# Performance work log

Measured on AMD Instinct MI355X. Metric: run time of the kernel, lower is better.

The kernel has to match this reference:

```python
import jax, jax.numpy as jnp
import numpy as np

B, T, H = 32, 2048, 1024
NEG = -1e9


def setup_inputs() -> dict:
    key = jax.random.key(0)
    ks = jax.random.split(key, 10)
    s = 1.0 / np.sqrt(H)
    return {
        "query": jax.random.normal(ks[0], (B, T, H), dtype=jnp.float32),
        "key_": jax.random.normal(ks[1], (B, T, H), dtype=jnp.float32),
        "value": jax.random.normal(ks[2], (B, T, H), dtype=jnp.float32),
        "lengths": jax.random.randint(ks[3], (B,), 1, T + 1),
        "Wq": jax.random.uniform(ks[4], (H, H), jnp.float32, -s, s),
        "bq": jax.random.uniform(ks[5], (H,), jnp.float32, -s, s),
        "Wk": jax.random.uniform(ks[6], (H, H), jnp.float32, -s, s),
        "bk": jax.random.uniform(ks[7], (H,), jnp.float32, -s, s),
        "Wz": jax.random.uniform(ks[8], (1, H), jnp.float32, -s, s),
        "bz": jax.random.uniform(ks[9], (1,), jnp.float32, -s, s),
    }


def reference(query, key_, value, lengths, Wq, bq, Wk, bk, Wz, bz):
    # projections: [B,T,H] @ [H,H]^T
    q = jnp.einsum("bth,oh->bto", query, Wq) + bq
    k = jnp.einsum("bth,oh->bto", key_, Wk) + bk
    # additive score -> [B,T,1]
    score = jnp.einsum("bth,oh->bto", jnp.tanh(q + k), Wz) + bz
    # mask positions t >= lengths[b]
    t_idx = jnp.arange(T)[None, :, None]  # [1,T,1]
    mask = t_idx >= lengths[:, None, None]  # [B,T,1]
    score = jnp.where(mask, NEG, score)
    att_weights = jax.nn.softmax(score, axis=1)  # [B,T,1]
    # weights^T [B,1,T] @ value [B,T,H] -> [B,1,H]
    att_value = jnp.einsum("bti,bth->bih", att_weights, value)
    return att_value, att_weights
```

## Files before the change

### kernel.cpp

```cpp
#include <hip/hip_runtime.h>
#include <hip/hip_bf16.h>

constexpr int TSEQ  = 2048;
constexpr int HDIM  = 1024;
constexpr int BATCH = 32;
constexpr int NPART = 16;
constexpr long ROWS = (long)BATCH * TSEQ;

constexpr int GBM = 256, GBN = 256, GBK = 64;
constexpr int GNT = (2 * HDIM) / GBK;

constexpr int BM = 128, BN = 128, BK = 64;
constexpr int NT = (2 * HDIM) / BK;

typedef __attribute__((ext_vector_type(8))) short bf16x8;
typedef __attribute__((ext_vector_type(8))) unsigned short u16x8;
typedef __attribute__((ext_vector_type(4))) float f32x4;

__device__ __forceinline__ unsigned short f2bf(float f) {
    union { float f; unsigned int u; } v; v.f = f;
    unsigned int r = v.u + 0x7FFFu + ((v.u >> 16) & 1u);
    return (unsigned short)(r >> 16);
}

__device__ __forceinline__ void gload16(const unsigned short* g, unsigned short* l) {
    __builtin_amdgcn_global_load_lds(
        (__attribute__((address_space(1))) void*)(g),
        (__attribute__((address_space(3))) void*)(l), 16, 0, 0);
}

__device__ __forceinline__ float fast_tanh(float x) {
    float e = __expf(2.0f * x);
    return 1.0f - 2.0f * __builtin_amdgcn_rcpf(e + 1.0f);
}

__global__ void convert_kernel(const float* __restrict__ q, const float* __restrict__ k,
                               const float* __restrict__ wq, const float* __restrict__ wk,
                               const int* __restrict__ lengths,
                               unsigned short* __restrict__ qb, unsigned short* __restrict__ kb,
                               unsigned short* __restrict__ wqb, unsigned short* __restrict__ wkb) {
    const long GQ = (ROWS * HDIM) / 8;
    const long GW = ((long)HDIM * HDIM) / 8;
    const long TOTAL = 2 * GQ + 2 * GW;
    const long stride = (long)gridDim.x * blockDim.x;
    for (long i = (long)blockIdx.x * blockDim.x + threadIdx.x; i < TOTAL; i += stride) {
        const float* src; unsigned short* dst; long off;
        if (i < 2 * GQ) {
            off = (i < GQ) ? i : i - GQ;
            const int row = (int)(off >> 7);
            if ((row & (TSEQ - 1)) >= lengths[row >> 11]) continue;
            src = (i < GQ) ? q : k;  dst = (i < GQ) ? qb : kb;
        } else if (i < 2 * GQ + GW) { src = wq; dst = wqb; off = i - 2 * GQ; }
        else                        { src = wk; dst = wkb; off = i - 2 * GQ - GW; }
        float4 v0 = *(const float4*)(src + off * 8);
        float4 v1 = *(const float4*)(src + off * 8 + 4);
        u16x8 o;
        o[0] = f2bf(v0.x); o[1] = f2bf(v0.y); o[2] = f2bf(v0.z); o[3] = f2bf(v0.w);
        o[4] = f2bf(v1.x); o[5] = f2bf(v1.y); o[6] = f2bf(v1.z); o[7] = f2bf(v1.w);
        *(u16x8*)(dst + off * 8) = o;
    }
}

__global__ __launch_bounds__(512, 2)
void score_gemm_256(const unsigned short* __restrict__ qb, const unsigned short* __restrict__ kb,
                    const unsigned short* __restrict__ wqb, const unsigned short* __restrict__ wkb,
                    const float* __restrict__ bq, const float* __restrict__ bk,
                    const float* __restrict__ Wz, const int* __restrict__ lengths,
                    float* __restrict__ scorePartial) {
    __shared__ unsigned short As[2 * 2 * 256 * 32];
    __shared__ unsigned short Bs[2 * 2 * 256 * 32];

    const int tid  = threadIdx.x;
    const int lane = tid & 63;
    const int wid  = tid >> 6;
    const int wr   = wid >> 2;
    const int wc   = wid & 3;

    const int lid = ((int)blockIdx.x & 7) * 128 + ((int)blockIdx.x >> 3);
    const int nb  = lid & 3;
    const int mb  = lid >> 2;
    const long rowBase = (long)mb * GBM;
    const int  colBase = nb * GBN;

    if ((int)(rowBase & (TSEQ - 1)) >= lengths[(int)(rowBase >> 11)]) return;

    const int frow = lane & 15;
    const int cs16 = (((lane >> 4) ^ ((frow >> 1) & 3)) << 4);
    const int sc8  = ((tid & 3) ^ ((tid >> 3) & 3)) * 8;

    f32x4 acc[8][4];
#pragma unroll
    for (int i = 0; i < 8; ++i)
#pragma unroll
        for (int j = 0; j < 4; ++j) acc[i][j] = (f32x4){0.f, 0.f, 0.f, 0.f};

    auto stage_half = [&](int n) {
        if (n >= 4 * GNT) return;
        const int tn   = n >> 2;
        const int part = n & 3;
        const int kh   = part >> 1;
        const int isB  = part & 1;
        const int kglob = tn * GBK + kh * 32;
        const unsigned short* src = (tn < 16) ? (isB ? wqb : qb) : (isB ? wkb : kb);
        const int ksrc = (tn < 16) ? kglob : (kglob - HDIM);
        const long rbase = isB ? (long)colBase : rowBase;
        unsigned short* lds = (isB ? Bs : As) + (tn & 1) * 16384 + kh * 8192;
#pragma unroll
        for (int j = 0; j < 2; ++j) {
            const int row = j * 128 + (tid >> 2);
            gload16(src + (rbase + row) * (long)HDIM + ksrc + sc8,
                    lds + j * 4096 + (tid << 3));
        }
    };

    bf16x8 afr[4], bfr[4];
    auto ldA = [&](int d, int kh, int mh) {
        const char* p = (const char*)As + d * 32768 + kh * 16384;
#pragma unroll
        for (int mi = 0; mi < 4; ++mi) {
            const int row = wr * 128 + (mh * 4 + mi) * 16 + frow;
            afr[mi] = *(const bf16x8*)(p + row * 64 + cs16);
        }
    };
    auto ldB = [&](int d, int kh) {
        const char* p = (const char*)Bs + d * 32768 + kh * 16384;
#pragma unroll
        for (int ni = 0; ni < 4; ++ni) {
            const int row = wc * 64 + ni * 16 + frow;
            bfr[ni] = *(const bf16x8*)(p + row * 64 + cs16);
        }
    };

#pragma unroll
    for (int n = 0; n < 6; ++n) stage_half(n);
    asm volatile("s_waitcnt vmcnt(4)" ::: "memory");
    __builtin_amdgcn_s_barrier();

    for (int t = 0; t < GNT; ++t) {
        const int d = t & 1;
#pragma unroll
        for (int q = 0; q < 4; ++q) {
            const int kh = q >> 1, mh = q & 1;
            if (mh == 0) ldB(d, kh);
            ldA(d, kh, mh);
            stage_half(4 * t + q + 6);
            __builtin_amdgcn_s_barrier();
            asm volatile("s_waitcnt lgkmcnt(0)" ::: "memory");
            __builtin_amdgcn_sched_barrier(0);
            __builtin_amdgcn_s_setprio(1);
#pragma unroll
            for (int mi = 0; mi < 4; ++mi)
#pragma unroll
                for (int ni = 0; ni < 4; ++ni)
                    acc[mh * 4 + mi][ni] = __builtin_amdgcn_mfma_f32_16x16x32_bf16(
                        afr[mi], bfr[ni], acc[mh * 4 + mi][ni], 0, 0, 0);
            __builtin_amdgcn_s_setprio(0);
            if (q == 3) {
                if (t < GNT - 2)       asm volatile("s_waitcnt vmcnt(4)" ::: "memory");
                else if (t == GNT - 2) asm volatile("s_waitcnt vmcnt(0)" ::: "memory");
            }
            __builtin_amdgcn_s_barrier();
        }
    }

    float bias[4], wz[4];
#pragma unroll
    for (int ni = 0; ni < 4; ++ni) {
        const int o = colBase + wc * 64 + ni * 16 + frow;
        bias[ni] = bq[o] + bk[o];
        wz[ni]   = Wz[o];
    }
#pragma unroll
    for (int mi = 0; mi < 8; ++mi) {
#pragma unroll
        for (int j = 0; j < 4; ++j) {
            float p = 0.f;
#pragma unroll
            for (int ni = 0; ni < 4; ++ni)
                p += fast_tanh(acc[mi][ni][j] + bias[ni]) * wz[ni];
#pragma unroll
            for (int off = 1; off < 16; off <<= 1) p += __shfl_xor(p, off);
            if (frow == 0) {
                long r = rowBase + wr * 128 + mi * 16 + (lane >> 4) * 4 + j;
                scorePartial[r * NPART + nb * 4 + wc] = p;
            }
        }
    }
}

__global__ __launch_bounds__(256, 2)
void score_gemm_fused(const float* __restrict__ query, const float* __restrict__ key_,
                      const float* __restrict__ Wq, const float* __restrict__ Wk,
                      const float* __restrict__ bq, const float* __restrict__ bk,
                      const float* __restrict__ Wz, const int* __restrict__ lengths,
                      float* __restrict__ scorePartial) {
    __shared__ unsigned short As[2][BM * BK];
    __shared__ unsigned short Bs[2][BN * BK];
    const int tid  = threadIdx.x;
    const int lane = tid & 63;
    const int wid  = tid >> 6;
    const int wr   = wid >> 1, wc = wid & 1;
    const int bid = blockIdx.x;
    const int nb  = bid & 7;
    const int mb  = bid >> 3;
    const long rowBase = (long)mb * BM;
    const int  colBase = nb * BN;
    if ((int)(rowBase & (TSEQ - 1)) >= lengths[(int)(rowBase >> 11)]) return;
    const int srow = tid >> 4;
    const int sc   = tid & 15;
    const int rA  = wr * 64 + (lane & 15);
    const int rB  = wc * 64 + (lane & 15);
    const int swz = (lane & 7) << 4;
    const int kb  = (lane >> 4) << 4;

    f32x4 acc[4][4];
#pragma unroll
    for (int i = 0; i < 4; i++)
#pragma unroll
        for (int j = 0; j < 4; j++) acc[i][j] = (f32x4){0.f, 0.f, 0.f, 0.f};

    float4 regA[8], regB[8];
    auto stage_load = [&](int kt) {
        const int kg = kt * BK;
        const float* baseA; const float* baseB; int koff;
        if (kg < HDIM) { baseA = query; baseB = Wq; koff = kg; }
        else           { baseA = key_;  baseB = Wk; koff = kg - HDIM; }
#pragma unroll
        for (int i = 0; i < 8; i++) {
            int row = i * 16 + srow;
            regA[i] = *(const float4*)(baseA + (rowBase + row) * (long)HDIM + koff + sc * 4);
            regB[i] = *(const float4*)(baseB + (long)(colBase + row) * HDIM + koff + sc * 4);
        }
    };
    auto stage_write = [&](int buf) {
#pragma unroll
        for (int i = 0; i < 8; i++) {
            int row = i * 16 + srow;
            int off = row * 128 + (((sc * 8)) ^ ((row & 7) << 4));
            ushort4 ha, hb;
            ha.x = f2bf(regA[i].x); ha.y = f2bf(regA[i].y);
            ha.z = f2bf(regA[i].z); ha.w = f2bf(regA[i].w);
            hb.x = f2bf(regB[i].x); hb.y = f2bf(regB[i].y);
            hb.z = f2bf(regB[i].z); hb.w = f2bf(regB[i].w);
            *(ushort4*)((char*)&As[buf][0] + off) = ha;
            *(ushort4*)((char*)&Bs[buf][0] + off) = hb;
        }
    };
    auto compute = [&](int buf) {
        const char* pA = (const char*)&As[buf][0];
        const char* pB = (const char*)&Bs[buf][0];
        bf16x8 a[4][2], b[4][2];
#pragma unroll
        for (int h = 0; h < 2; h++) {
#pragma unroll
            for (int mi = 0; mi < 4; mi++)
                a[mi][h] = *(const bf16x8*)(pA + (((rA + mi * 16) * 128 + h * 64 + kb) ^ swz));
#pragma unroll
            for (int ni = 0; ni < 4; ni++)
                b[ni][h] = *(const bf16x8*)(pB + (((rB + ni * 16) * 128 + h * 64 + kb) ^ swz));
        }
#pragma unroll
        for (int h = 0; h < 2; h++)
#pragma unroll
            for (int mi = 0; mi < 4; mi++)
#pragma unroll
                for (int ni = 0; ni < 4; ni++)
                    acc[mi][ni] = __builtin_amdgcn_mfma_f32_16x16x32_bf16(
                        a[mi][h], b[ni][h], acc[mi][ni], 0, 0, 0);
    };

    stage_load(0);
    stage_write(0);
    __syncthreads();
    int buf = 0;
    for (int kt = 1; kt < NT; ++kt) {
        stage_load(kt);
        compute(buf);
        stage_write(buf ^ 1);
        __syncthreads();
        buf ^= 1;
    }
    compute(buf);

    float bias[4], wz[4];
#pragma unroll
    for (int ni = 0; ni < 4; ni++) {
        int o = colBase + wc * 64 + ni * 16 + (lane & 15);
        bias[ni] = bq[o] + bk[o];
        wz[ni]   = Wz[o];
    }
#pragma unroll
    for (int mi = 0; mi < 4; mi++) {
#pragma unroll
        for (int j = 0; j < 4; j++) {
            float p = 0.f;
#pragma unroll
            for (int ni = 0; ni < 4; ni++) {
                float s = acc[mi][ni][j] + bias[ni];
                p += fast_tanh(s) * wz[ni];
            }
#pragma unroll
            for (int off = 1; off < 16; off <<= 1) p += __shfl_xor(p, off);
            if ((lane & 15) == 0) {
                long r = rowBase + wr * 64 + mi * 16 + (lane >> 4) * 4 + j;
                scorePartial[r * NPART + nb * 2 + wc] = p;
            }
        }
    }
}

__global__ void softmax_kernel(const float* __restrict__ sp, const float* __restrict__ bzp,
                               const int* __restrict__ lengths,
                               float* __restrict__ w_out, float* __restrict__ w_ws) {
    const int b = blockIdx.x;
    const int tid = threadIdx.x;
    const int len = lengths[b];
    const float bz = bzp[0];
    float sv[8];
    float m = -3.0e38f;
#pragma unroll
    for (int i = 0; i < 8; i++) {
        int t = i * 256 + tid;
        const float4* p = (const float4*)(sp + ((long)b * TSEQ + t) * NPART);
        float s;
        if (t >= len) {
            s = -1e9f;
        } else {
            float4 a = p[0], c = p[1], d = p[2], e = p[3];
            s = (a.x + a.y + a.z + a.w) + (c.x + c.y + c.z + c.w) +
                (d.x + d.y + d.z + d.w) + (e.x + e.y + e.z + e.w) + bz;
        }
        sv[i] = s;
        m = fmaxf(m, s);
    }
    __shared__ float redm[4];
    __shared__ float reds[4];
    for (int off = 32; off; off >>= 1) m = fmaxf(m, __shfl_xor(m, off));
    if ((tid & 63) == 0) redm[tid >> 6] = m;
    __syncthreads();
    m = fmaxf(fmaxf(redm[0], redm[1]), fmaxf(redm[2], redm[3]));
    float sum = 0.f;
    float ev[8];
#pragma unroll
    for (int i = 0; i < 8; i++) {
        ev[i] = expf(sv[i] - m);
        sum += ev[i];
    }
    for (int off = 32; off; off >>= 1) sum += __shfl_xor(sum, off);
    if ((tid & 63) == 0) reds[tid >> 6] = sum;
    __syncthreads();
    sum = reds[0] + reds[1] + reds[2] + reds[3];
    const float inv = 1.0f / sum;
#pragma unroll
    for (int i = 0; i < 8; i++) {
        int t = i * 256 + tid;
        float w = ev[i] * inv;
        w_out[(long)b * TSEQ + t] = w;
        w_ws[(long)b * TSEQ + t] = w;
    }
}

__global__ void pv_partial(const float* __restrict__ w, const float* __restrict__ value,
                           const int* __restrict__ lengths, float* __restrict__ part) {
    const int ntc = gridDim.x;
    const int tchunk = TSEQ / ntc;
    const int tc = blockIdx.x;
    const int hc = blockIdx.y;
    const int b  = blockIdx.z;
    const int tid = threadIdx.x;
    const int h = hc * 512 + tid * 4;
    float* dst = part + ((long)(b * ntc + tc)) * HDIM + h;
    if (tc * tchunk >= lengths[b]) {
        *(float4*)dst = (float4){0.f, 0.f, 0.f, 0.f};
        return;
    }
    __shared__ float sw[128];
    if (tid < tchunk) sw[tid] = w[(long)b * TSEQ + tc * tchunk + tid];
    __syncthreads();
    float4 acc = {0.f, 0.f, 0.f, 0.f};
    const float* vbase = value + ((long)b * TSEQ + tc * tchunk) * HDIM + h;
#pragma unroll 4
    for (int tt = 0; tt < tchunk; ++tt) {
        float4 v = *(const float4*)(vbase + (long)tt * HDIM);
        float wv = sw[tt];
        acc.x += wv * v.x; acc.y += wv * v.y;
        acc.z += wv * v.z; acc.w += wv * v.w;
    }
    *(float4*)dst = acc;
}

__global__ void pv_reduce(const float* __restrict__ part, float* __restrict__ out, int ntc) {
    const int b = blockIdx.x;
    const int tid = threadIdx.x;
    const int h = tid * 4;
    float4 acc = {0.f, 0.f, 0.f, 0.f};
    for (int tc = 0; tc < ntc; ++tc) {
        float4 v = *(const float4*)(part + ((long)(b * ntc + tc)) * HDIM + h);
        acc.x += v.x; acc.y += v.y; acc.z += v.z; acc.w += v.w;
    }
    *(float4*)(out + (long)b * HDIM + h) = acc;
}

extern "C" void kernel_launch(void* const* d_in, const int* in_sizes, int n_in,
                              void* d_out, int out_size, void* d_ws, size_t ws_size,
                              hipStream_t stream) {
    const float* query   = (const float*)d_in[0];
    const float* key_    = (const float*)d_in[1];
    const float* value   = (const float*)d_in[2];
    const int*   lengths = (const int*)d_in[3];
    const float* Wq = (const float*)d_in[4];
    const float* bq = (const float*)d_in[5];
    const float* Wk = (const float*)d_in[6];
    const float* bk = (const float*)d_in[7];
    const float* Wz = (const float*)d_in[8];
    const float* bz = (const float*)d_in[9];
    float* out = (float*)d_out;

    const long QB_B  = ROWS * HDIM * 2;
    const long WB_B  = (long)HDIM * HDIM * 2;
    const long SP_B  = ROWS * NPART * 4;
    const long WW_B  = ROWS * 4;
    const long P2_B  = (long)BATCH * 32 * HDIM * 4;
    const long NEED  = 2 * QB_B + 2 * WB_B + SP_B + WW_B + P2_B;

    if ((long)ws_size >= NEED) {
        char* w = (char*)d_ws;
        unsigned short* qb  = (unsigned short*)w;            w += QB_B;
        unsigned short* kb  = (unsigned short*)w;            w += QB_B;
        unsigned short* wqb = (unsigned short*)w;            w += WB_B;
        unsigned short* wkb = (unsigned short*)w;            w += WB_B;
        float* sp   = (float*)w;                             w += SP_B;
        float* wbuf = (float*)w;                             w += WW_B;
        float* p2   = (float*)w;

        convert_kernel<<<dim3(4096), dim3(256), 0, stream>>>(
            query, key_, Wq, Wk, lengths, qb, kb, wqb, wkb);
        score_gemm_256<<<dim3(1024), dim3(512), 0, stream>>>(
            qb, kb, wqb, wkb, bq, bk, Wz, lengths, sp);
        softmax_kernel<<<dim3(BATCH), dim3(256), 0, stream>>>(
            sp, bz, lengths, out + BATCH * HDIM, wbuf);
        pv_partial<<<dim3(32, 2, BATCH), dim3(128), 0, stream>>>(wbuf, value, lengths, p2);
        pv_reduce<<<dim3(BATCH), dim3(256), 0, stream>>>(p2, out, 32);
    } else {
        float* sp   = (float*)d_ws;
        float* wbuf = sp + ROWS * NPART;
        float* p2   = wbuf + ROWS;
        score_gemm_fused<<<dim3(4096), dim3(256), 0, stream>>>(
            query, key_, Wq, Wk, bq, bk, Wz, lengths, sp);
        softmax_kernel<<<dim3(BATCH), dim3(256), 0, stream>>>(
            sp, bz, lengths, out + BATCH * HDIM, wbuf);
        pv_partial<<<dim3(16, 2, BATCH), dim3(128), 0, stream>>>(wbuf, value, lengths, p2);
        pv_reduce<<<dim3(BATCH), dim3(256), 0, stream>>>(p2, out, 16);
    }
}
```

Baseline: 333.3 us.

## Shrink score GEMM tile to 128x256 with triple-buffered LDS and length-balanced block mapping

Replaces the 256x256 tile score GEMM with a 128x256 tile variant launched on twice as many blocks, using a three-stage LDS ring with K-halves of 32 and higher occupancy (launch bounds 4 blocks). Block indices are remapped so each XCD group interleaves batches and intra-sequence row tiles, balancing variable-length masked work across CUs. Smaller tiles cut wasted compute past sequence lengths and improve occupancy, at the cost of lower arithmetic intensity per block (more B reloads) and more blocks.

```diff
diff --git a/kernel.cpp b/kernel.cpp
--- a/kernel.cpp
+++ b/kernel.cpp
@@ -6,9 +6,6 @@
 constexpr int BATCH = 32;
 constexpr int NPART = 16;
 constexpr long ROWS = (long)BATCH * TSEQ;
-
-constexpr int GBM = 256, GBN = 256, GBK = 64;
-constexpr int GNT = (2 * HDIM) / GBK;
 
 constexpr int BM = 128, BN = 128, BK = 64;
 constexpr int NT = (2 * HDIM) / BK;
@@ -61,14 +58,14 @@
     }
 }
 
-__global__ __launch_bounds__(512, 2)
-void score_gemm_256(const unsigned short* __restrict__ qb, const unsigned short* __restrict__ kb,
+__global__ __launch_bounds__(512, 4)
+void score_gemm_128(const unsigned short* __restrict__ qb, const unsigned short* __restrict__ kb,
                     const unsigned short* __restrict__ wqb, const unsigned short* __restrict__ wkb,
                     const float* __restrict__ bq, const float* __restrict__ bk,
                     const float* __restrict__ Wz, const int* __restrict__ lengths,
                     float* __restrict__ scorePartial) {
-    __shared__ unsigned short As[2 * 2 * 256 * 32];
-    __shared__ unsigned short Bs[2 * 2 * 256 * 32];
+    __shared__ unsigned short As[3 * 128 * 32];
+    __shared__ unsigned short Bs[3 * 256 * 32];
 
     const int tid  = threadIdx.x;
     const int lane = tid & 63;
@@ -76,91 +73,73 @@
     const int wr   = wid >> 2;
     const int wc   = wid & 3;
 
-    const int lid = ((int)blockIdx.x & 7) * 128 + ((int)blockIdx.x >> 3);
-    const int nb  = lid & 3;
-    const int mb  = lid >> 2;
-    const long rowBase = (long)mb * GBM;
-    const int  colBase = nb * GBN;
-
-    if ((int)(rowBase & (TSEQ - 1)) >= lengths[(int)(rowBase >> 11)]) return;
+    const int x   = (int)blockIdx.x & 7;
+    const int s   = (int)blockIdx.x >> 3;
+    const int bat = s & 31;
+    const int nb  = (s >> 5) & 3;
+    const int ip  = s >> 7;
+    const int intra = ((x << 1) + ip + bat) & 15;
+    const long rowBase = ((long)bat << 11) + (long)intra * 128;
+    const int  colBase = nb * 256;
+
+    if (intra * 128 >= lengths[bat]) return;
 
     const int frow = lane & 15;
     const int cs16 = (((lane >> 4) ^ ((frow >> 1) & 3)) << 4);
     const int sc8  = ((tid & 3) ^ ((tid >> 3) & 3)) * 8;
 
-    f32x4 acc[8][4];
-#pragma unroll
-    for (int i = 0; i < 8; ++i)
+    f32x4 acc[4][4];
+#pragma unroll
+    for (int i = 0; i < 4; ++i)
 #pragma unroll
         for (int j = 0; j < 4; ++j) acc[i][j] = (f32x4){0.f, 0.f, 0.f, 0.f};
 
-    auto stage_half = [&](int n) {
-        if (n >= 4 * GNT) return;
-        const int tn   = n >> 2;
-        const int part = n & 3;
-        const int kh   = part >> 1;
-        const int isB  = part & 1;
-        const int kglob = tn * GBK + kh * 32;
-        const unsigned short* src = (tn < 16) ? (isB ? wqb : qb) : (isB ? wkb : kb);
-        const int ksrc = (tn < 16) ? kglob : (kglob - HDIM);
-        const long rbase = isB ? (long)colBase : rowBase;
-        unsigned short* lds = (isB ? Bs : As) + (tn & 1) * 16384 + kh * 8192;
-#pragma unroll
-        for (int j = 0; j < 2; ++j) {
-            const int row = j * 128 + (tid >> 2);
-            gload16(src + (rbase + row) * (long)HDIM + ksrc + sc8,
-                    lds + j * 4096 + (tid << 3));
+    auto stage_pair = [&](int n) {
+        const int tn  = n >> 1;
+        const unsigned short* asrc = (tn < 16) ? qb : kb;
+        const unsigned short* bsrc = (tn < 16) ? wqb : wkb;
+        const int ksrc = (tn & 15) * 64 + (n & 1) * 32 + sc8;
+        const int buf = n % 3;
+        gload16(asrc + (rowBase + (tid >> 2)) * (long)HDIM + ksrc,
+                As + buf * 4096 + (tid << 3));
+#pragma unroll
+        for (int jj = 0; jj < 2; ++jj) {
+            const int row = jj * 128 + (tid >> 2);
+            gload16(bsrc + (long)(colBase + row) * HDIM + ksrc,
+                    Bs + buf * 8192 + jj * 4096 + (tid << 3));
         }
     };
 
-    bf16x8 afr[4], bfr[4];
-    auto ldA = [&](int d, int kh, int mh) {
-        const char* p = (const char*)As + d * 32768 + kh * 16384;
-#pragma unroll
-        for (int mi = 0; mi < 4; ++mi) {
-            const int row = wr * 128 + (mh * 4 + mi) * 16 + frow;
-            afr[mi] = *(const bf16x8*)(p + row * 64 + cs16);
-        }
-    };
-    auto ldB = [&](int d, int kh) {
-        const char* p = (const char*)Bs + d * 32768 + kh * 16384;
-#pragma unroll
-        for (int ni = 0; ni < 4; ++ni) {
-            const int row = wc * 64 + ni * 16 + frow;
-            bfr[ni] = *(const bf16x8*)(p + row * 64 + cs16);
-        }
-    };
-
-#pragma unroll
-    for (int n = 0; n < 6; ++n) stage_half(n);
-    asm volatile("s_waitcnt vmcnt(4)" ::: "memory");
+    stage_pair(0);
+    stage_pair(1);
+    asm volatile("s_waitcnt vmcnt(3)" ::: "memory");
     __builtin_amdgcn_s_barrier();
 
-    for (int t = 0; t < GNT; ++t) {
-        const int d = t & 1;
-#pragma unroll
-        for (int q = 0; q < 4; ++q) {
-            const int kh = q >> 1, mh = q & 1;
-            if (mh == 0) ldB(d, kh);
-            ldA(d, kh, mh);
-            stage_half(4 * t + q + 6);
-            __builtin_amdgcn_s_barrier();
-            asm volatile("s_waitcnt lgkmcnt(0)" ::: "memory");
-            __builtin_amdgcn_sched_barrier(0);
-            __builtin_amdgcn_s_setprio(1);
-#pragma unroll
-            for (int mi = 0; mi < 4; ++mi)
-#pragma unroll
-                for (int ni = 0; ni < 4; ++ni)
-                    acc[mh * 4 + mi][ni] = __builtin_amdgcn_mfma_f32_16x16x32_bf16(
-                        afr[mi], bfr[ni], acc[mh * 4 + mi][ni], 0, 0, 0);
-            __builtin_amdgcn_s_setprio(0);
-            if (q == 3) {
-                if (t < GNT - 2)       asm volatile("s_waitcnt vmcnt(4)" ::: "memory");
-                else if (t == GNT - 2) asm volatile("s_waitcnt vmcnt(0)" ::: "memory");
-            }
-            __builtin_amdgcn_s_barrier();
-        }
+    for (int h = 0; h < 64; ++h) {
+        if (h + 2 < 64) stage_pair(h + 2);
+        const int buf = h % 3;
+        const char* pA = (const char*)As + buf * 8192;
+        const char* pB = (const char*)Bs + buf * 16384;
+        bf16x8 afr[4], bfr[4];
+#pragma unroll
+        for (int mi = 0; mi < 4; ++mi)
+            afr[mi] = *(const bf16x8*)(pA + (wr * 64 + mi * 16 + frow) * 64 + cs16);
+#pragma unroll
+        for (int ni = 0; ni < 4; ++ni)
+            bfr[ni] = *(const bf16x8*)(pB + (wc * 64 + ni * 16 + frow) * 64 + cs16);
+        asm volatile("s_waitcnt lgkmcnt(0)" ::: "memory");
+        __builtin_amdgcn_sched_barrier(0);
+        __builtin_amdgcn_s_setprio(1);
+#pragma unroll
+        for (int mi = 0; mi < 4; ++mi)
+#pragma unroll
+            for (int ni = 0; ni < 4; ++ni)
+                acc[mi][ni] = __builtin_amdgcn_mfma_f32_16x16x32_bf16(
+                    afr[mi], bfr[ni], acc[mi][ni], 0, 0, 0);
+        __builtin_amdgcn_s_setprio(0);
+        if (h <= 61)      asm volatile("s_waitcnt vmcnt(3)" ::: "memory");
+        else if (h == 62) asm volatile("s_waitcnt vmcnt(0)" ::: "memory");
+        __builtin_amdgcn_s_barrier();
     }
 
     float bias[4], wz[4];
@@ -171,7 +150,7 @@
         wz[ni]   = Wz[o];
     }
 #pragma unroll
-    for (int mi = 0; mi < 8; ++mi) {
+    for (int mi = 0; mi < 4; ++mi) {
 #pragma unroll
         for (int j = 0; j < 4; ++j) {
             float p = 0.f;
@@ -181,7 +160,7 @@
 #pragma unroll
             for (int off = 1; off < 16; off <<= 1) p += __shfl_xor(p, off);
             if (frow == 0) {
-                long r = rowBase + wr * 128 + mi * 16 + (lane >> 4) * 4 + j;
+                long r = rowBase + wr * 64 + mi * 16 + (lane >> 4) * 4 + j;
                 scorePartial[r * NPART + nb * 4 + wc] = p;
             }
         }
@@ -435,7 +414,7 @@
 
         convert_kernel<<<dim3(4096), dim3(256), 0, stream>>>(
             query, key_, Wq, Wk, lengths, qb, kb, wqb, wkb);
-        score_gemm_256<<<dim3(1024), dim3(512), 0, stream>>>(
+        score_gemm_128<<<dim3(2048), dim3(512), 0, stream>>>(
             qb, kb, wqb, wkb, bq, bk, Wz, lengths, sp);
         softmax_kernel<<<dim3(BATCH), dim3(256), 0, stream>>>(
             sp, bz, lengths, out + BATCH * HDIM, wbuf);
```

Result: slower. 367.1 us (+10.1%).
